# Kernel optimization log

Hardware: AMD Instinct MI355X
Metric: run time of the kernel (lower is better)

Reference implementation:

```python
import jax, jax.numpy as jnp
import numpy as np
from jax import lax

P = 16      # n_features
H = 24      # hidden size (hard-coded in module)
B = 8192
T = 168


def setup_inputs() -> dict:
    key = jax.random.key(0)
    ks = jax.random.split(key, 8)
    s_ih = 1.0 / np.sqrt(H)
    return {
        "x": jax.random.normal(ks[0], (B, T, P), dtype=jnp.float32),
        # PyTorch LSTM params: gate order [i, f, g, o], uniform(-1/sqrt(H), 1/sqrt(H))
        "W_ih": jax.random.uniform(ks[1], (4 * H, P), jnp.float32, -s_ih, s_ih),
        "W_hh": jax.random.uniform(ks[2], (4 * H, H), jnp.float32, -s_ih, s_ih),
        "b_ih": jax.random.uniform(ks[3], (4 * H,), jnp.float32, -s_ih, s_ih),
        "b_hh": jax.random.uniform(ks[4], (4 * H,), jnp.float32, -s_ih, s_ih),
        "W_lin": jax.random.uniform(ks[5], (H, H), jnp.float32, -s_ih, s_ih),
        "b_lin": jax.random.uniform(ks[6], (H,), jnp.float32, -s_ih, s_ih),
    }


def _lstm_last_h(x, W_ih, W_hh, b_ih, b_hh):
    # Precompute input-side gate pre-activations for all timesteps: [B, T, 4H]
    xg = jnp.einsum("btp,gp->btg", x, W_ih) + (b_ih + b_hh)
    W_hh_T = W_hh.T  # [H, 4H]
    Bsz = x.shape[0]
    h0 = jnp.zeros((Bsz, H), dtype=x.dtype)
    c0 = jnp.zeros((Bsz, H), dtype=x.dtype)

    def step(carry, xt):
        h, c = carry
        g = xt + h @ W_hh_T  # [B, 4H]
        i = jax.nn.sigmoid(g[:, 0 * H:1 * H])
        f = jax.nn.sigmoid(g[:, 1 * H:2 * H])
        gg = jnp.tanh(g[:, 2 * H:3 * H])
        o = jax.nn.sigmoid(g[:, 3 * H:4 * H])
        c = f * c + i * gg
        h = o * jnp.tanh(c)
        return (h, c), None

    (h_last, _), _ = lax.scan(step, (h0, c0), jnp.swapaxes(xg, 0, 1))
    return h_last  # [B, H]


def reference(x, W_ih, W_hh, b_ih, b_hh, W_lin, b_lin):
    h_last = _lstm_last_h(x, W_ih, W_hh, b_ih, b_hh)
    # tanh over LSTM outputs, then linear head on the last timestep
    out = jnp.tanh(h_last) @ W_lin.T + b_lin  # [B, H]
    return out.reshape(out.shape[0], -1, 1)   # [B, 24, 1]
```

## Files before the change

kernel.cpp:

```cpp
#include <hip/hip_runtime.h>


#define T_STEPS 168
#define P_FEAT  16
#define TCH     84
#define NB      16
#define BPAD    24
#define BSTR    (TCH * 16 + BPAD)

typedef _Float16 half8 __attribute__((ext_vector_type(8)));
typedef _Float16 h2    __attribute__((ext_vector_type(2)));
typedef float    f32x4 __attribute__((ext_vector_type(4)));

__device__ __forceinline__ float rcp_fast(float x) {
#if __has_builtin(__builtin_amdgcn_rcpf)
    return __builtin_amdgcn_rcpf(x);
#else
    return 1.0f / x;
#endif
}
__device__ __forceinline__ float exp2_fast(float x) {
#if __has_builtin(__builtin_amdgcn_exp2f)
    return __builtin_amdgcn_exp2f(x);
#else
    return exp2f(x);
#endif
}
__device__ __forceinline__ float tanh_f(float x) {
    return 1.0f - 2.0f * rcp_fast(1.0f + exp2_fast(x * 2.88539008f));
}
__device__ __forceinline__ h2 pack2(float a, float b) {
    h2 r; r.x = (_Float16)a; r.y = (_Float16)b; return r;
}

__global__ __launch_bounds__(512, 4) void lstm_8w(
    const float* __restrict__ x,
    const float* __restrict__ W_ih,
    const float* __restrict__ W_hh,
    const float* __restrict__ b_ih,
    const float* __restrict__ b_hh,
    const float* __restrict__ W_lin,
    const float* __restrict__ b_lin,
    float* __restrict__ out)
{
    __shared__ __align__(16) _Float16 xs16[NB * BSTR];
    __shared__ __align__(16) _Float16 hx[2][4][NB][8];
    __shared__ __align__(16) _Float16 zblk[16];
    __shared__ __align__(16) float    thbuf[NB][24];

    const int tid  = threadIdx.x;
    const int w    = tid >> 6;
    const int lane = tid & 63;
    const int n    = lane & 15;
    const int q    = lane >> 4;

    float* wstage = reinterpret_cast<float*>(xs16);
    for (int idx = tid; idx < 96 * 40; idx += 512) {
        const int j = idx / 40;
        const int k = idx - j * 40;
        wstage[idx] = (k < 24) ? W_hh[j * 24 + k] : W_ih[j * 16 + (k - 24)];
    }
    __syncthreads();

    half8 A1, A2;
    f32x4 biasf;
    {
        const int mt = w;
        const int p  = n;
        const bool vrow = (p < 12);
        const int grow = vrow ? ((p & 3) * 24 + 8 * (p >> 2) + mt) : 0;
        #pragma unroll
        for (int j = 0; j < 8; j++) {
            const int k = q * 8 + j;
            A1[j] = (vrow && k < 24) ? (_Float16)wstage[grow * 40 + k]      : (_Float16)0.0f;
            A2[j] = (vrow && k < 16) ? (_Float16)wstage[grow * 40 + 24 + k] : (_Float16)0.0f;
        }
        #pragma unroll
        for (int r = 0; r < 4; r++) {
            const int u = 8 * q + mt;
            biasf[r] = (q < 3) ? (b_ih[r * 24 + u] + b_hh[r * 24 + u]) : 0.0f;
        }
    }
    {
        unsigned* hz = reinterpret_cast<unsigned*>(&hx[0][0][0][0]);
        for (int i = tid; i < 512; i += 512) hz[i] = 0u;
        if (tid < 8) reinterpret_cast<unsigned*>(zblk)[tid] = 0u;
    }
    __syncthreads();

    float c  = 0.0f;
    float hv = 0.0f;

    const float4* xsrc = reinterpret_cast<const float4*>(x)
                       + (size_t)(blockIdx.x * NB) * (T_STEPS * P_FEAT / 4);

    const _Float16* xrowbase = (q < 2) ? &xs16[n * BSTR + q * 8] : zblk;
    const int xstep = (q < 2) ? 16 : 0;

    int bufp = 0;
    for (int ch = 0; ch < 2; ch++) {
        for (int i = 0; i < 11; i++) {
            const int m = tid + 512 * i;
            if (m < 5376) {
                const int b   = m / 336;
                const int rem = m - b * 336;
                const float4 v = xsrc[(size_t)b * 672 + ch * 336 + rem];
                h2* dst = reinterpret_cast<h2*>(xs16) + b * (BSTR / 2) + rem * 2;
                dst[0] = pack2(v.x, v.y);
                dst[1] = pack2(v.z, v.w);
            }
        }
        __syncthreads();

        f32x4 gx;
        {
            const half8 B2 = *reinterpret_cast<const half8*>(xrowbase);
            gx = __builtin_amdgcn_mfma_f32_16x16x32_f16(A2, B2, biasf, 0, 0, 0);
        }

        for (int t = 0; t < TCH; t++) {
            const half8 B1 = *reinterpret_cast<const half8*>(&hx[bufp][q][n][0]);
            const int tn = (t + 1 < TCH) ? t + 1 : 0;
            const half8 B2n = *reinterpret_cast<const half8*>(xrowbase + tn * xstep);

            f32x4 g = __builtin_amdgcn_mfma_f32_16x16x32_f16(A1, B1, gx, 0, 0, 0);
            gx = __builtin_amdgcn_mfma_f32_16x16x32_f16(A2, B2n, biasf, 0, 0, 0);

            {
                const float Y  = exp2_fast(g[0] * -1.44269504f);
                const float X  = exp2_fast(g[1] * -1.44269504f);
                const float Z  = exp2_fast(g[2] *  2.88539008f);
                const float V  = exp2_fast(g[3] * -1.44269504f);
                const float ax = 1.0f + X;
                const float ay = 1.0f + Y;
                const float az = 1.0f + Z;
                const float num = c * ay * az + ax * (Z - 1.0f);
                const float cn  = num * rcp_fast(ax * ay * az);
                c = cn;
                const float W  = exp2_fast(fminf(cn, 18.0f) * 2.88539008f);
                hv = (W - 1.0f) * rcp_fast((1.0f + V) * (1.0f + W));
            }

            if (q < 3) hx[1 - bufp][q][n][w] = (_Float16)hv;
            bufp ^= 1;
            __syncthreads();
        }
    }

    if (q < 3) thbuf[n][8 * q + w] = tanh_f(hv);
    __syncthreads();

    if (q < 3) {
        const int batch = blockIdx.x * NB + n;
        const int u = 8 * q + w;
        const float* wl = &W_lin[u * 24];
        float acc = b_lin[u];
        #pragma unroll
        for (int k = 0; k < 24; k++) acc = fmaf(thbuf[n][k], wl[k], acc);
        out[(size_t)batch * 24 + u] = acc;
    }
}

extern "C" void kernel_launch(void* const* d_in, const int* in_sizes, int n_in,
                              void* d_out, int out_size, void* d_ws, size_t ws_size,
                              hipStream_t stream) {
    const float* x     = (const float*)d_in[0];
    const float* W_ih  = (const float*)d_in[1];
    const float* W_hh  = (const float*)d_in[2];
    const float* b_ih  = (const float*)d_in[3];
    const float* b_hh  = (const float*)d_in[4];
    const float* W_lin = (const float*)d_in[5];
    const float* b_lin = (const float*)d_in[6];
    float* out = (float*)d_out;

    const int B = in_sizes[0] / (T_STEPS * P_FEAT);
    dim3 grid(B / NB), block(512);
    lstm_8w<<<grid, block, 0, stream>>>(x, W_ih, W_hh, b_ih, b_hh, W_lin, b_lin, out);
}
```

Measured before the change: 195.9 us.

## Interleave two batch chains per block and stream x directly from global memory

```diff
diff --git a/kernel.cpp b/kernel.cpp
--- a/kernel.cpp
+++ b/kernel.cpp
@@ -3,13 +3,9 @@
 
 #define T_STEPS 168
 #define P_FEAT  16
-#define TCH     84
-#define NB      16
-#define BPAD    24
-#define BSTR    (TCH * 16 + BPAD)
+#define NBW     32
 
 typedef _Float16 half8 __attribute__((ext_vector_type(8)));
-typedef _Float16 h2    __attribute__((ext_vector_type(2)));
 typedef float    f32x4 __attribute__((ext_vector_type(4)));
 
 __device__ __forceinline__ float rcp_fast(float x) {
@@ -29,11 +25,11 @@
 __device__ __forceinline__ float tanh_f(float x) {
     return 1.0f - 2.0f * rcp_fast(1.0f + exp2_fast(x * 2.88539008f));
 }
-__device__ __forceinline__ h2 pack2(float a, float b) {
-    h2 r; r.x = (_Float16)a; r.y = (_Float16)b; return r;
+__device__ __forceinline__ void soft_barrier() {
+    asm volatile("s_waitcnt lgkmcnt(0)\n\ts_barrier" ::: "memory");
 }
 
-__global__ __launch_bounds__(512, 4) void lstm_8w(
+__global__ __launch_bounds__(512, 2) void lstm_2c(
     const float* __restrict__ x,
     const float* __restrict__ W_ih,
     const float* __restrict__ W_hh,
@@ -43,121 +39,137 @@
     const float* __restrict__ b_lin,
     float* __restrict__ out)
 {
-    __shared__ __align__(16) _Float16 xs16[NB * BSTR];
-    __shared__ __align__(16) _Float16 hx[2][4][NB][8];
-    __shared__ __align__(16) _Float16 zblk[16];
-    __shared__ __align__(16) float    thbuf[NB][24];
+    __shared__ __align__(16) _Float16 hx[2][2][4][16][8];
+    __shared__ __align__(16) float    thbuf[2][16][25];
 
     const int tid  = threadIdx.x;
     const int w    = tid >> 6;
     const int lane = tid & 63;
     const int n    = lane & 15;
     const int q    = lane >> 4;
+    const int batchA = blockIdx.x * NBW + n;
+    const int batchB = batchA + 16;
 
-    float* wstage = reinterpret_cast<float*>(xs16);
-    for (int idx = tid; idx < 96 * 40; idx += 512) {
-        const int j = idx / 40;
-        const int k = idx - j * 40;
-        wstage[idx] = (k < 24) ? W_hh[j * 24 + k] : W_ih[j * 16 + (k - 24)];
+    half8 WA1, WA2;
+    f32x4 biasf;
+    {
+        const int p = n;
+        const bool vrow = (p < 12);
+        const int grow = vrow ? ((p & 3) * 24 + 8 * (p >> 2) + w) : 0;
+        #pragma unroll
+        for (int j = 0; j < 8; j++) {
+            const int k = 8 * q + j;
+            WA1[j] = (vrow && k < 24) ? (_Float16)W_hh[grow * 24 + k] : (_Float16)0.0f;
+            WA2[j] = (vrow && k < 16) ? (_Float16)W_ih[grow * 16 + k] : (_Float16)0.0f;
+        }
+        const int u = 8 * q + w;
+        #pragma unroll
+        for (int r = 0; r < 4; r++)
+            biasf[r] = (q < 3) ? (b_ih[r * 24 + u] + b_hh[r * 24 + u]) : 0.0f;
+    }
+
+    {
+        unsigned* hz = reinterpret_cast<unsigned*>(&hx[0][0][0][0][0]);
+        hz[tid] = 0u;
+        hz[tid + 512] = 0u;
     }
     __syncthreads();
 
-    half8 A1, A2;
-    f32x4 biasf;
+    const float* xrowA = x + (size_t)batchA * (T_STEPS * P_FEAT) + 8 * q;
+    const float* xrowB = x + (size_t)batchB * (T_STEPS * P_FEAT) + 8 * q;
+
+    auto xload = [&](const float* xr, int t, float4& r0, float4& r1) {
+        if (q < 2) {
+            const float4* p = reinterpret_cast<const float4*>(xr + (size_t)t * P_FEAT);
+            r0 = p[0];
+            r1 = p[1];
+        }
+    };
+    auto mkB2 = [&](const float4& r0, const float4& r1) -> half8 {
+        half8 b = {};
+        if (q < 2) {
+            b[0] = (_Float16)r0.x; b[1] = (_Float16)r0.y;
+            b[2] = (_Float16)r0.z; b[3] = (_Float16)r0.w;
+            b[4] = (_Float16)r1.x; b[5] = (_Float16)r1.y;
+            b[6] = (_Float16)r1.z; b[7] = (_Float16)r1.w;
+        }
+        return b;
+    };
+    auto cell = [&](const f32x4& g, float& c, float& hv) {
+        const float Y  = exp2_fast(g[0] * -1.44269504f);
+        const float X  = exp2_fast(g[1] * -1.44269504f);
+        const float Z  = exp2_fast(g[2] *  2.88539008f);
+        const float V  = exp2_fast(g[3] * -1.44269504f);
+        const float ax = 1.0f + X;
+        const float ay = 1.0f + Y;
+        const float az = 1.0f + Z;
+        const float num = c * ay * az + ax * (Z - 1.0f);
+        const float cn  = num * rcp_fast(ax * ay * az);
+        c = cn;
+        const float Wt = exp2_fast(fminf(cn, 18.0f) * 2.88539008f);
+        hv = (Wt - 1.0f) * rcp_fast((1.0f + V) * (1.0f + Wt));
+    };
+
+    float cA = 0.0f, cB = 0.0f, hvA = 0.0f, hvB = 0.0f;
+    f32x4 gxA, gxB;
+    int bufp = 0;
+
+    float4 xae0, xae1, xbe0, xbe1;
+    float4 xao0, xao1, xbo0, xbo1;
+
     {
-        const int mt = w;
-        const int p  = n;
-        const bool vrow = (p < 12);
-        const int grow = vrow ? ((p & 3) * 24 + 8 * (p >> 2) + mt) : 0;
-        #pragma unroll
-        for (int j = 0; j < 8; j++) {
-            const int k = q * 8 + j;
-            A1[j] = (vrow && k < 24) ? (_Float16)wstage[grow * 40 + k]      : (_Float16)0.0f;
-            A2[j] = (vrow && k < 16) ? (_Float16)wstage[grow * 40 + 24 + k] : (_Float16)0.0f;
+        float4 t0a0 = {0,0,0,0}, t0a1 = {0,0,0,0}, t0b0 = {0,0,0,0}, t0b1 = {0,0,0,0};
+        xload(xrowA, 0, t0a0, t0a1);
+        xload(xrowB, 0, t0b0, t0b1);
+        xload(xrowA, 1, xae0, xae1);
+        xload(xrowB, 1, xbe0, xbe1);
+        xload(xrowA, 2, xao0, xao1);
+        xload(xrowB, 2, xbo0, xbo1);
+        gxA = __builtin_amdgcn_mfma_f32_16x16x32_f16(WA2, mkB2(t0a0, t0a1), biasf, 0, 0, 0);
+        gxB = __builtin_amdgcn_mfma_f32_16x16x32_f16(WA2, mkB2(t0b0, t0b1), biasf, 0, 0, 0);
+    }
+
+    auto one_t = [&](float4& a0, float4& a1, float4& b0, float4& b1, int tload) {
+        const half8 hA = *reinterpret_cast<const half8*>(&hx[bufp][0][q][n][0]);
+        const half8 hB = *reinterpret_cast<const half8*>(&hx[bufp][1][q][n][0]);
+        f32x4 gA = __builtin_amdgcn_mfma_f32_16x16x32_f16(WA1, hA, gxA, 0, 0, 0);
+        f32x4 gB = __builtin_amdgcn_mfma_f32_16x16x32_f16(WA1, hB, gxB, 0, 0, 0);
+        gxA = __builtin_amdgcn_mfma_f32_16x16x32_f16(WA2, mkB2(a0, a1), biasf, 0, 0, 0);
+        gxB = __builtin_amdgcn_mfma_f32_16x16x32_f16(WA2, mkB2(b0, b1), biasf, 0, 0, 0);
+        xload(xrowA, tload, a0, a1);
+        xload(xrowB, tload, b0, b1);
+        cell(gA, cA, hvA);
+        cell(gB, cB, hvB);
+        if (q < 3) {
+            hx[1 - bufp][0][q][n][w] = (_Float16)hvA;
+            hx[1 - bufp][1][q][n][w] = (_Float16)hvB;
         }
-        #pragma unroll
-        for (int r = 0; r < 4; r++) {
-            const int u = 8 * q + mt;
-            biasf[r] = (q < 3) ? (b_ih[r * 24 + u] + b_hh[r * 24 + u]) : 0.0f;
-        }
+        bufp ^= 1;
+        soft_barrier();
+    };
+
+    for (int t = 0; t < T_STEPS; t += 2) {
+        one_t(xae0, xae1, xbe0, xbe1, (t + 3 < T_STEPS) ? t + 3 : 0);
+        one_t(xao0, xao1, xbo0, xbo1, (t + 4 < T_STEPS) ? t + 4 : 0);
     }
-    {
-        unsigned* hz = reinterpret_cast<unsigned*>(&hx[0][0][0][0]);
-        for (int i = tid; i < 512; i += 512) hz[i] = 0u;
-        if (tid < 8) reinterpret_cast<unsigned*>(zblk)[tid] = 0u;
+
+    if (q < 3) {
+        thbuf[0][n][8 * q + w] = tanh_f(hvA);
+        thbuf[1][n][8 * q + w] = tanh_f(hvB);
     }
     __syncthreads();
 
-    float c  = 0.0f;
-    float hv = 0.0f;
-
-    const float4* xsrc = reinterpret_cast<const float4*>(x)
-                       + (size_t)(blockIdx.x * NB) * (T_STEPS * P_FEAT / 4);
-
-    const _Float16* xrowbase = (q < 2) ? &xs16[n * BSTR + q * 8] : zblk;
-    const int xstep = (q < 2) ? 16 : 0;
-
-    int bufp = 0;
-    for (int ch = 0; ch < 2; ch++) {
-        for (int i = 0; i < 11; i++) {
-            const int m = tid + 512 * i;
-            if (m < 5376) {
-                const int b   = m / 336;
-                const int rem = m - b * 336;
-                const float4 v = xsrc[(size_t)b * 672 + ch * 336 + rem];
-                h2* dst = reinterpret_cast<h2*>(xs16) + b * (BSTR / 2) + rem * 2;
-                dst[0] = pack2(v.x, v.y);
-                dst[1] = pack2(v.z, v.w);
-            }
-        }
-        __syncthreads();
-
-        f32x4 gx;
-        {
-            const half8 B2 = *reinterpret_cast<const half8*>(xrowbase);
-            gx = __builtin_amdgcn_mfma_f32_16x16x32_f16(A2, B2, biasf, 0, 0, 0);
-        }
-
-        for (int t = 0; t < TCH; t++) {
-            const half8 B1 = *reinterpret_cast<const half8*>(&hx[bufp][q][n][0]);
-            const int tn = (t + 1 < TCH) ? t + 1 : 0;
-            const half8 B2n = *reinterpret_cast<const half8*>(xrowbase + tn * xstep);
-
-            f32x4 g = __builtin_amdgcn_mfma_f32_16x16x32_f16(A1, B1, gx, 0, 0, 0);
-            gx = __builtin_amdgcn_mfma_f32_16x16x32_f16(A2, B2n, biasf, 0, 0, 0);
-
-            {
-                const float Y  = exp2_fast(g[0] * -1.44269504f);
-                const float X  = exp2_fast(g[1] * -1.44269504f);
-                const float Z  = exp2_fast(g[2] *  2.88539008f);
-                const float V  = exp2_fast(g[3] * -1.44269504f);
-                const float ax = 1.0f + X;
-                const float ay = 1.0f + Y;
-                const float az = 1.0f + Z;
-                const float num = c * ay * az + ax * (Z - 1.0f);
-                const float cn  = num * rcp_fast(ax * ay * az);
-                c = cn;
-                const float W  = exp2_fast(fminf(cn, 18.0f) * 2.88539008f);
-                hv = (W - 1.0f) * rcp_fast((1.0f + V) * (1.0f + W));
-            }
-
-            if (q < 3) hx[1 - bufp][q][n][w] = (_Float16)hv;
-            bufp ^= 1;
-            __syncthreads();
-        }
-    }
-
-    if (q < 3) thbuf[n][8 * q + w] = tanh_f(hv);
-    __syncthreads();
-
     if (q < 3) {
-        const int batch = blockIdx.x * NB + n;
         const int u = 8 * q + w;
         const float* wl = &W_lin[u * 24];
-        float acc = b_lin[u];
+        float accA = b_lin[u], accB = accA;
         #pragma unroll
-        for (int k = 0; k < 24; k++) acc = fmaf(thbuf[n][k], wl[k], acc);
-        out[(size_t)batch * 24 + u] = acc;
+        for (int k = 0; k < 24; k++) {
+            accA = fmaf(thbuf[0][n][k], wl[k], accA);
+            accB = fmaf(thbuf[1][n][k], wl[k], accB);
+        }
+        out[(size_t)batchA * 24 + u] = accA;
+        out[(size_t)batchB * 24 + u] = accB;
     }
 }
 
@@ -174,6 +186,6 @@
     float* out = (float*)d_out;
 
     const int B = in_sizes[0] / (T_STEPS * P_FEAT);
-    dim3 grid(B / NB), block(512);
-    lstm_8w<<<grid, block, 0, stream>>>(x, W_ih, W_hh, b_ih, b_hh, W_lin, b_lin, out);
+    dim3 grid(B / NBW), block(512);
+    lstm_2c<<<grid, block, 0, stream>>>(x, W_ih, W_hh, b_ih, b_hh, W_lin, b_lin, out);
 }
```

After: 242.7 us. 1.24x slower.

## Stream x directly from global into registers with prefetch, drop LDS staging

Applied to the files above, without the earlier changes.

```diff
diff --git a/kernel.cpp b/kernel.cpp
--- a/kernel.cpp
+++ b/kernel.cpp
@@ -3,13 +3,9 @@
 
 #define T_STEPS 168
 #define P_FEAT  16
-#define TCH     84
 #define NB      16
-#define BPAD    24
-#define BSTR    (TCH * 16 + BPAD)
 
 typedef _Float16 half8 __attribute__((ext_vector_type(8)));
-typedef _Float16 h2    __attribute__((ext_vector_type(2)));
 typedef float    f32x4 __attribute__((ext_vector_type(4)));
 
 __device__ __forceinline__ float rcp_fast(float x) {
@@ -29,11 +25,11 @@
 __device__ __forceinline__ float tanh_f(float x) {
     return 1.0f - 2.0f * rcp_fast(1.0f + exp2_fast(x * 2.88539008f));
 }
-__device__ __forceinline__ h2 pack2(float a, float b) {
-    h2 r; r.x = (_Float16)a; r.y = (_Float16)b; return r;
+__device__ __forceinline__ void soft_barrier() {
+    asm volatile("s_waitcnt lgkmcnt(0)\n\ts_barrier" ::: "memory");
 }
 
-__global__ __launch_bounds__(512, 4) void lstm_8w(
+__global__ __launch_bounds__(512, 2) void lstm_gx(
     const float* __restrict__ x,
     const float* __restrict__ W_ih,
     const float* __restrict__ W_hh,
@@ -43,9 +39,7 @@
     const float* __restrict__ b_lin,
     float* __restrict__ out)
 {
-    __shared__ __align__(16) _Float16 xs16[NB * BSTR];
     __shared__ __align__(16) _Float16 hx[2][4][NB][8];
-    __shared__ __align__(16) _Float16 zblk[16];
     __shared__ __align__(16) float    thbuf[NB][24];
 
     const int tid  = threadIdx.x;
@@ -53,105 +47,102 @@
     const int lane = tid & 63;
     const int n    = lane & 15;
     const int q    = lane >> 4;
-
-    float* wstage = reinterpret_cast<float*>(xs16);
-    for (int idx = tid; idx < 96 * 40; idx += 512) {
-        const int j = idx / 40;
-        const int k = idx - j * 40;
-        wstage[idx] = (k < 24) ? W_hh[j * 24 + k] : W_ih[j * 16 + (k - 24)];
-    }
-    __syncthreads();
+    const int batch = blockIdx.x * NB + n;
 
     half8 A1, A2;
     f32x4 biasf;
     {
-        const int mt = w;
         const int p  = n;
         const bool vrow = (p < 12);
-        const int grow = vrow ? ((p & 3) * 24 + 8 * (p >> 2) + mt) : 0;
+        const int grow = vrow ? ((p & 3) * 24 + 8 * (p >> 2) + w) : 0;
         #pragma unroll
         for (int j = 0; j < 8; j++) {
             const int k = q * 8 + j;
-            A1[j] = (vrow && k < 24) ? (_Float16)wstage[grow * 40 + k]      : (_Float16)0.0f;
-            A2[j] = (vrow && k < 16) ? (_Float16)wstage[grow * 40 + 24 + k] : (_Float16)0.0f;
+            A1[j] = (vrow && k < 24) ? (_Float16)W_hh[grow * 24 + k] : (_Float16)0.0f;
+            A2[j] = (vrow && k < 16) ? (_Float16)W_ih[grow * 16 + k] : (_Float16)0.0f;
         }
         #pragma unroll
         for (int r = 0; r < 4; r++) {
-            const int u = 8 * q + mt;
+            const int u = 8 * q + w;
             biasf[r] = (q < 3) ? (b_ih[r * 24 + u] + b_hh[r * 24 + u]) : 0.0f;
         }
     }
     {
         unsigned* hz = reinterpret_cast<unsigned*>(&hx[0][0][0][0]);
-        for (int i = tid; i < 512; i += 512) hz[i] = 0u;
-        if (tid < 8) reinterpret_cast<unsigned*>(zblk)[tid] = 0u;
+        if (tid < 512) hz[tid] = 0u;
     }
     __syncthreads();
 
     float c  = 0.0f;
     float hv = 0.0f;
 
-    const float4* xsrc = reinterpret_cast<const float4*>(x)
-                       + (size_t)(blockIdx.x * NB) * (T_STEPS * P_FEAT / 4);
+    const float* xrow = x + (size_t)batch * (T_STEPS * P_FEAT) + 8 * q;
 
-    const _Float16* xrowbase = (q < 2) ? &xs16[n * BSTR + q * 8] : zblk;
-    const int xstep = (q < 2) ? 16 : 0;
+    auto xload = [&](int t, float4& r0, float4& r1) {
+        if (q < 2) {
+            const float4* p = reinterpret_cast<const float4*>(xrow + (size_t)t * P_FEAT);
+            r0 = p[0];
+            r1 = p[1];
+        }
+    };
+    auto mkB2 = [&](const float4& r0, const float4& r1) -> half8 {
+        half8 b = {};
+        if (q < 2) {
+            b[0] = (_Float16)r0.x; b[1] = (_Float16)r0.y;
+            b[2] = (_Float16)r0.z; b[3] = (_Float16)r0.w;
+            b[4] = (_Float16)r1.x; b[5] = (_Float16)r1.y;
+            b[6] = (_Float16)r1.z; b[7] = (_Float16)r1.w;
+        }
+        return b;
+    };
 
+    f32x4 gx;
     int bufp = 0;
-    for (int ch = 0; ch < 2; ch++) {
-        for (int i = 0; i < 11; i++) {
-            const int m = tid + 512 * i;
-            if (m < 5376) {
-                const int b   = m / 336;
-                const int rem = m - b * 336;
-                const float4 v = xsrc[(size_t)b * 672 + ch * 336 + rem];
-                h2* dst = reinterpret_cast<h2*>(xs16) + b * (BSTR / 2) + rem * 2;
-                dst[0] = pack2(v.x, v.y);
-                dst[1] = pack2(v.z, v.w);
-            }
+
+    float4 xe0 = {0,0,0,0}, xe1 = {0,0,0,0};
+    float4 xo0 = {0,0,0,0}, xo1 = {0,0,0,0};
+
+    {
+        float4 t00 = {0,0,0,0}, t01 = {0,0,0,0};
+        xload(0, t00, t01);
+        xload(1, xe0, xe1);
+        xload(2, xo0, xo1);
+        gx = __builtin_amdgcn_mfma_f32_16x16x32_f16(A2, mkB2(t00, t01), biasf, 0, 0, 0);
+    }
+
+    auto one_t = [&](float4& b0, float4& b1, int tload) {
+        const half8 B1 = *reinterpret_cast<const half8*>(&hx[bufp][q][n][0]);
+        f32x4 g = __builtin_amdgcn_mfma_f32_16x16x32_f16(A1, B1, gx, 0, 0, 0);
+        gx = __builtin_amdgcn_mfma_f32_16x16x32_f16(A2, mkB2(b0, b1), biasf, 0, 0, 0);
+        xload(tload, b0, b1);
+        {
+            const float Y  = exp2_fast(g[0] * -1.44269504f);
+            const float X  = exp2_fast(g[1] * -1.44269504f);
+            const float Z  = exp2_fast(g[2] *  2.88539008f);
+            const float V  = exp2_fast(g[3] * -1.44269504f);
+            const float ax = 1.0f + X;
+            const float ay = 1.0f + Y;
+            const float az = 1.0f + Z;
+            const float num = c * ay * az + ax * (Z - 1.0f);
+            const float cn  = num * rcp_fast(ax * ay * az);
+            c = cn;
+            const float W  = exp2_fast(fminf(cn, 18.0f) * 2.88539008f);
+            hv = (W - 1.0f) * rcp_fast((1.0f + V) * (1.0f + W));
         }
-        __syncthreads();
+        if (q < 3) hx[1 - bufp][q][n][w] = (_Float16)hv;
+        bufp ^= 1;
+        soft_barrier();
+    };
 
-        f32x4 gx;
-        {
-            const half8 B2 = *reinterpret_cast<const half8*>(xrowbase);
-            gx = __builtin_amdgcn_mfma_f32_16x16x32_f16(A2, B2, biasf, 0, 0, 0);
-        }
-
-        for (int t = 0; t < TCH; t++) {
-            const half8 B1 = *reinterpret_cast<const half8*>(&hx[bufp][q][n][0]);
-            const int tn = (t + 1 < TCH) ? t + 1 : 0;
-            const half8 B2n = *reinterpret_cast<const half8*>(xrowbase + tn * xstep);
-
-            f32x4 g = __builtin_amdgcn_mfma_f32_16x16x32_f16(A1, B1, gx, 0, 0, 0);
-            gx = __builtin_amdgcn_mfma_f32_16x16x32_f16(A2, B2n, biasf, 0, 0, 0);
-
-            {
-                const float Y  = exp2_fast(g[0] * -1.44269504f);
-                const float X  = exp2_fast(g[1] * -1.44269504f);
-                const float Z  = exp2_fast(g[2] *  2.88539008f);
-                const float V  = exp2_fast(g[3] * -1.44269504f);
-                const float ax = 1.0f + X;
-                const float ay = 1.0f + Y;
-                const float az = 1.0f + Z;
-                const float num = c * ay * az + ax * (Z - 1.0f);
-                const float cn  = num * rcp_fast(ax * ay * az);
-                c = cn;
-                const float W  = exp2_fast(fminf(cn, 18.0f) * 2.88539008f);
-                hv = (W - 1.0f) * rcp_fast((1.0f + V) * (1.0f + W));
-            }
-
-            if (q < 3) hx[1 - bufp][q][n][w] = (_Float16)hv;
-            bufp ^= 1;
-            __syncthreads();
-        }
+    for (int t = 0; t < T_STEPS; t += 2) {
+        one_t(xe0, xe1, (t + 3 < T_STEPS) ? t + 3 : 0);
+        one_t(xo0, xo1, (t + 4 < T_STEPS) ? t + 4 : 0);
     }
 
     if (q < 3) thbuf[n][8 * q + w] = tanh_f(hv);
     __syncthreads();
 
     if (q < 3) {
-        const int batch = blockIdx.x * NB + n;
         const int u = 8 * q + w;
         const float* wl = &W_lin[u * 24];
         float acc = b_lin[u];
@@ -175,5 +166,5 @@
 
     const int B = in_sizes[0] / (T_STEPS * P_FEAT);
     dim3 grid(B / NB), block(512);
-    lstm_8w<<<grid, block, 0, stream>>>(x, W_ih, W_hh, b_ih, b_hh, W_lin, b_lin, out);
+    lstm_gx<<<grid, block, 0, stream>>>(x, W_ih, W_hh, b_ih, b_hh, W_lin, b_lin, out);
 }
```

Measured after the change: 220.5 us. 1.13x slower.

## Remap hidden units to six waves per 16-batch group, two groups per block

Applied to the files above, without the earlier changes.

```diff
diff --git a/kernel.cpp b/kernel.cpp
--- a/kernel.cpp
+++ b/kernel.cpp
@@ -4,7 +4,7 @@
 #define T_STEPS 168
 #define P_FEAT  16
 #define TCH     84
-#define NB      16
+#define NB      32
 #define BPAD    24
 #define BSTR    (TCH * 16 + BPAD)
 
@@ -33,7 +33,7 @@
     h2 r; r.x = (_Float16)a; r.y = (_Float16)b; return r;
 }
 
-__global__ __launch_bounds__(512, 4) void lstm_8w(
+__global__ __launch_bounds__(768, 3) void lstm_6t(
     const float* __restrict__ x,
     const float* __restrict__ W_ih,
     const float* __restrict__ W_hh,
@@ -44,18 +44,21 @@
     float* __restrict__ out)
 {
     __shared__ __align__(16) _Float16 xs16[NB * BSTR];
-    __shared__ __align__(16) _Float16 hx[2][4][NB][8];
+    __shared__ __align__(16) _Float16 hx[2][2][4][16][8];
     __shared__ __align__(16) _Float16 zblk[16];
-    __shared__ __align__(16) float    thbuf[NB][24];
+    __shared__ __align__(16) float    thbuf[2][16][25];
 
     const int tid  = threadIdx.x;
     const int w    = tid >> 6;
     const int lane = tid & 63;
     const int n    = lane & 15;
     const int q    = lane >> 4;
+    const int cc   = (w >= 6);
+    const int tau  = w - 6 * cc;
+    const int batch = blockIdx.x * NB + 16 * cc + n;
 
     float* wstage = reinterpret_cast<float*>(xs16);
-    for (int idx = tid; idx < 96 * 40; idx += 512) {
+    for (int idx = tid; idx < 96 * 40; idx += 768) {
         const int j = idx / 40;
         const int k = idx - j * 40;
         wstage[idx] = (k < 24) ? W_hh[j * 24 + k] : W_ih[j * 16 + (k - 24)];
@@ -65,25 +68,21 @@
     half8 A1, A2;
     f32x4 biasf;
     {
-        const int mt = w;
-        const int p  = n;
-        const bool vrow = (p < 12);
-        const int grow = vrow ? ((p & 3) * 24 + 8 * (p >> 2) + mt) : 0;
+        const int grow = (n & 3) * 24 + 6 * (n >> 2) + tau;
         #pragma unroll
         for (int j = 0; j < 8; j++) {
+            A1[j] = (j < 6) ? (_Float16)wstage[grow * 40 + 6 * q + j] : (_Float16)0.0f;
             const int k = q * 8 + j;
-            A1[j] = (vrow && k < 24) ? (_Float16)wstage[grow * 40 + k]      : (_Float16)0.0f;
-            A2[j] = (vrow && k < 16) ? (_Float16)wstage[grow * 40 + 24 + k] : (_Float16)0.0f;
+            A2[j] = (k < 16) ? (_Float16)wstage[grow * 40 + 24 + k] : (_Float16)0.0f;
         }
+        const int u = 6 * q + tau;
         #pragma unroll
-        for (int r = 0; r < 4; r++) {
-            const int u = 8 * q + mt;
-            biasf[r] = (q < 3) ? (b_ih[r * 24 + u] + b_hh[r * 24 + u]) : 0.0f;
-        }
+        for (int r = 0; r < 4; r++)
+            biasf[r] = b_ih[r * 24 + u] + b_hh[r * 24 + u];
     }
     {
-        unsigned* hz = reinterpret_cast<unsigned*>(&hx[0][0][0][0]);
-        for (int i = tid; i < 512; i += 512) hz[i] = 0u;
+        unsigned* hz = reinterpret_cast<unsigned*>(&hx[0][0][0][0][0]);
+        if (tid < 512) { hz[tid] = 0u; hz[tid + 512] = 0u; }
         if (tid < 8) reinterpret_cast<unsigned*>(zblk)[tid] = 0u;
     }
     __syncthreads();
@@ -94,21 +93,19 @@
     const float4* xsrc = reinterpret_cast<const float4*>(x)
                        + (size_t)(blockIdx.x * NB) * (T_STEPS * P_FEAT / 4);
 
-    const _Float16* xrowbase = (q < 2) ? &xs16[n * BSTR + q * 8] : zblk;
+    const _Float16* xrowbase = (q < 2) ? &xs16[(16 * cc + n) * BSTR + q * 8] : zblk;
     const int xstep = (q < 2) ? 16 : 0;
 
     int bufp = 0;
     for (int ch = 0; ch < 2; ch++) {
-        for (int i = 0; i < 11; i++) {
-            const int m = tid + 512 * i;
-            if (m < 5376) {
-                const int b   = m / 336;
-                const int rem = m - b * 336;
-                const float4 v = xsrc[(size_t)b * 672 + ch * 336 + rem];
-                h2* dst = reinterpret_cast<h2*>(xs16) + b * (BSTR / 2) + rem * 2;
-                dst[0] = pack2(v.x, v.y);
-                dst[1] = pack2(v.z, v.w);
-            }
+        for (int i = 0; i < 14; i++) {
+            const int m   = tid + 768 * i;
+            const int b   = m / 336;
+            const int rem = m - b * 336;
+            const float4 v = xsrc[(size_t)b * 672 + ch * 336 + rem];
+            h2* dst = reinterpret_cast<h2*>(xs16) + b * (BSTR / 2) + rem * 2;
+            dst[0] = pack2(v.x, v.y);
+            dst[1] = pack2(v.z, v.w);
         }
         __syncthreads();
 
@@ -119,7 +116,7 @@
         }
 
         for (int t = 0; t < TCH; t++) {
-            const half8 B1 = *reinterpret_cast<const half8*>(&hx[bufp][q][n][0]);
+            const half8 B1 = *reinterpret_cast<const half8*>(&hx[bufp][cc][q][n][0]);
             const int tn = (t + 1 < TCH) ? t + 1 : 0;
             const half8 B2n = *reinterpret_cast<const half8*>(xrowbase + tn * xstep);
 
@@ -141,22 +138,21 @@
                 hv = (W - 1.0f) * rcp_fast((1.0f + V) * (1.0f + W));
             }
 
-            if (q < 3) hx[1 - bufp][q][n][w] = (_Float16)hv;
+            hx[1 - bufp][cc][q][n][tau] = (_Float16)hv;
             bufp ^= 1;
             __syncthreads();
         }
     }
 
-    if (q < 3) thbuf[n][8 * q + w] = tanh_f(hv);
+    thbuf[cc][n][6 * q + tau] = tanh_f(hv);
     __syncthreads();
 
-    if (q < 3) {
-        const int batch = blockIdx.x * NB + n;
-        const int u = 8 * q + w;
+    {
+        const int u = 6 * q + tau;
         const float* wl = &W_lin[u * 24];
         float acc = b_lin[u];
         #pragma unroll
-        for (int k = 0; k < 24; k++) acc = fmaf(thbuf[n][k], wl[k], acc);
+        for (int k = 0; k < 24; k++) acc = fmaf(thbuf[cc][n][k], wl[k], acc);
         out[(size_t)batch * 24 + u] = acc;
     }
 }
@@ -174,6 +170,6 @@
     float* out = (float*)d_out;
 
     const int B = in_sizes[0] / (T_STEPS * P_FEAT);
-    dim3 grid(B / NB), block(512);
-    lstm_8w<<<grid, block, 0, stream>>>(x, W_ih, W_hh, b_ih, b_hh, W_lin, b_lin, out);
+    dim3 grid(B / NB), block(768);
+    lstm_6t<<<grid, block, 0, stream>>>(x, W_ih, W_hh, b_ih, b_hh, W_lin, b_lin, out);
 }
```

After: 194.5 us. About the same (-0.7%).
